# Performance work log

Hardware: AMD Instinct MI355X
Metric: run time of the kernel (lower is better)

Reference implementation:

```python
import jax, jax.numpy as jnp
import numpy as np

D = 1024
H = 16
DH = D // H

def setup_inputs() -> dict:
    key = jax.random.key(0)
    k1, k2, k3, k4 = jax.random.split(key, 4)
    x = jax.random.normal(k1, (4, 2048, D), dtype=jnp.float32)
    # qkv_linear: Linear(D, D, bias=False); weight stored as (out, in) torch-style
    w_qkv = jax.random.normal(k2, (D, D), dtype=jnp.float32) * (1.0 / np.sqrt(D))
    # final linear: Linear(D, D) with bias
    w_out = jax.random.normal(k3, (D, D), dtype=jnp.float32) * (1.0 / np.sqrt(D))
    b_out = jax.random.normal(k4, (D,), dtype=jnp.float32) * 0.01
    return {"x": x, "w_qkv": w_qkv, "w_out": w_out, "b_out": b_out}

def reference(x, w_qkv, w_out, b_out):
    B, S, E = x.shape
    # Same projection used for Q, K, V (faithful to original module)
    qkv = jnp.einsum('bse,de->bsd', x, w_qkv)           # [B,S,D]
    qkv = qkv.reshape(B, S, H, DH).transpose(0, 2, 1, 3)  # [B,H,S,Dh]
    q = k = v = qkv
    scale = DH ** -0.5
    attn = jnp.einsum('bhqd,bhkd->bhqk', q, k) * scale   # [B,H,S,S]
    attn = jax.nn.softmax(attn, axis=-1)
    out = jnp.einsum('bhqk,bhkd->bhqd', attn, v)         # [B,H,S,Dh]
    out = out.transpose(0, 2, 1, 3).reshape(B, S, E)
    return jnp.einsum('bse,de->bsd', out, w_out) + b_out
```

## Files before the change

kernel.cpp:

```cpp
#include <hip/hip_runtime.h>
#include <hip/hip_bf16.h>
#include <stdint.h>

typedef unsigned short u16;
typedef unsigned int   u32;
typedef unsigned long long u64;
typedef __bf16 bf16x8 __attribute__((ext_vector_type(8)));
typedef float  f32x4  __attribute__((ext_vector_type(4)));
typedef short  s16x4  __attribute__((ext_vector_type(4)));

#define D_MODEL 1024
#define NH 16
#define DHEAD 64
#define BB 4
#define SS 2048
#define MM (BB*SS)

__device__ __forceinline__ u16 f2bf(float f) {
    unsigned int u = __float_as_uint(f);
    u += 0x7fffu + ((u >> 16) & 1u);
    return (u16)(u >> 16);
}
__device__ __forceinline__ float bf2f(u16 s) {
    return __uint_as_float(((unsigned int)s) << 16);
}
__device__ __forceinline__ u32 pkbf(float a, float b) {
    __hip_bfloat162 h = __float22bfloat162_rn(make_float2(a, b));
    return *(u32*)&h;
}

union U8 {
    uint4 q;
    u16   v[8];
    bf16x8 f;
};
union B8 { u32 w[4]; bf16x8 f; };
union V8 { s16x4 h[2]; bf16x8 f; };

#define N4X (MM * D_MODEL / 4)
#define N4W (D_MODEL * D_MODEL / 4)
__global__ __launch_bounds__(256) void cvt_all_kernel(const float* __restrict__ x,
                                                      const float* __restrict__ wq,
                                                      const float* __restrict__ wo,
                                                      u16* __restrict__ xb,
                                                      u16* __restrict__ wqb,
                                                      u16* __restrict__ wob) {
    int i = blockIdx.x * 256 + threadIdx.x;
    const float* s; u16* d; int off;
    if (i < N4X)            { s = x;  d = xb;  off = i; }
    else if (i < N4X + N4W) { s = wq; d = wqb; off = i - N4X; }
    else                    { s = wo; d = wob; off = i - N4X - N4W; }
    float4 f = ((const float4*)s)[off];
    u32 o[2] = { pkbf(f.x, f.y), pkbf(f.z, f.w) };
    ((uint2*)d)[off] = *(const uint2*)o;
}

template <bool PERMUTE_OUT>
__device__ __forceinline__ void gemm_body(const u16* __restrict__ A,
                                          const u16* __restrict__ Bt,
                                          const float* __restrict__ Bo,
                                          u16* __restrict__ Cq, u16* __restrict__ CqT,
                                          float* __restrict__ Out)
{
    __shared__ __align__(16) u16 As[128*64];
    __shared__ __align__(16) u16 Bs[128*64];

    const int tid  = threadIdx.x;
    const int wave = tid >> 6;
    const int lane = tid & 63;
    const int quad = lane >> 4;
    const int l16  = lane & 15;
    const int dsw = blockIdx.x;
    const int sl  = dsw >> 3;
    const int bm  = ((sl >> 3) << 3) + (dsw & 7);
    const int bn  = sl & 7;
    const int wm = wave >> 1, wn = wave & 1;

    f32x4 acc[4][4] = {};

    const int rp = tid >> 3;
    const int ch = tid & 7;
    const int sc = ch ^ (rp & 7);

    const u16* Ab = A  + (size_t)(bm * 128 + rp) * D_MODEL + sc * 8;
    const u16* Bb = Bt + (size_t)(bn * 128 + rp) * D_MODEL + sc * 8;
    const int xr = l16 & 7;

    for (int k0 = 0; k0 < D_MODEL; k0 += 64) {
#pragma unroll
        for (int p = 0; p < 4; ++p) {
            __builtin_amdgcn_global_load_lds(
                (__attribute__((address_space(1))) void*)(Ab + (size_t)(32*p) * D_MODEL + k0),
                (__attribute__((address_space(3))) void*)(As + p*2048 + tid*8), 16, 0, 0);
            __builtin_amdgcn_global_load_lds(
                (__attribute__((address_space(1))) void*)(Bb + (size_t)(32*p) * D_MODEL + k0),
                (__attribute__((address_space(3))) void*)(Bs + p*2048 + tid*8), 16, 0, 0);
        }
        __syncthreads();

#pragma unroll
        for (int ks = 0; ks < 2; ++ks) {
            bf16x8 af[4], bfr[4];
#pragma unroll
            for (int t = 0; t < 4; ++t)
                af[t] = *(const bf16x8*)(const void*)(
                    As + (wm*64 + t*16 + l16)*64 + (((ks*4 + quad) ^ xr) * 8));
#pragma unroll
            for (int t = 0; t < 4; ++t)
                bfr[t] = *(const bf16x8*)(const void*)(
                    Bs + (wn*64 + t*16 + l16)*64 + (((ks*4 + quad) ^ xr) * 8));
#pragma unroll
            for (int i = 0; i < 4; ++i)
#pragma unroll
                for (int j = 0; j < 4; ++j)
                    acc[i][j] = __builtin_amdgcn_mfma_f32_16x16x32_bf16(af[i], bfr[j], acc[i][j], 0, 0, 0);
        }
        __syncthreads();
    }

    const int rowbase = bm*128 + wm*64;
    const int colbase = bn*128 + wn*64;
    if (PERMUTE_OUT) {
#pragma unroll
        for (int j = 0; j < 4; ++j) {
            const int col = colbase + j*16 + l16;
            const int h = col >> 6, dh = col & 63;
#pragma unroll
            for (int i = 0; i < 4; ++i) {
                const int row0 = rowbase + i*16 + quad*4;
                const int b = row0 >> 11, s0 = row0 & (SS - 1);
#pragma unroll
                for (int r = 0; r < 4; ++r)
                    Cq[(((size_t)(b*NH + h))*SS + s0 + r)*DHEAD + dh] = f2bf(acc[i][j][r]);
                u64 w = (u64)pkbf(acc[i][j][0], acc[i][j][1])
                      | ((u64)pkbf(acc[i][j][2], acc[i][j][3]) << 32);
                *(u64*)(CqT + ((size_t)((b*NH + h)*DHEAD + dh))*SS + s0) = w;
            }
        }
    } else {
#pragma unroll
        for (int j = 0; j < 4; ++j) {
            const int col = colbase + j*16 + l16;
            const float bias = Bo[col];
#pragma unroll
            for (int i = 0; i < 4; ++i) {
#pragma unroll
                for (int r = 0; r < 4; ++r) {
                    const int row = rowbase + i*16 + quad*4 + r;
                    Out[(size_t)row * D_MODEL + col] = acc[i][j][r] + bias;
                }
            }
        }
    }
}

__global__ __launch_bounds__(256) void gemm_qkv_kernel(const u16* __restrict__ A,
                                                       const u16* __restrict__ Bt,
                                                       u16* __restrict__ Cq,
                                                       u16* __restrict__ CqT) {
    gemm_body<true>(A, Bt, nullptr, Cq, CqT, nullptr);
}

__global__ __launch_bounds__(256) void gemm_out_kernel(const u16* __restrict__ A,
                                                       const u16* __restrict__ Bt,
                                                       const float* __restrict__ Bo,
                                                       float* __restrict__ Out) {
    gemm_body<false>(A, Bt, Bo, nullptr, nullptr, Out);
}

__global__ __launch_bounds__(256, 2) void attn_kernel(const u16* __restrict__ qkv,
                                                      const u16* __restrict__ qkvT,
                                                      u16* __restrict__ outb)
{
    __shared__ __align__(16) u16 Ks[2*2048];
    __shared__ __align__(16) u16 Vt[2*2048];

    const int tid  = threadIdx.x;
    const int wave = tid >> 6;
    const int lane = tid & 63;
    const int quad = lane >> 4;
    const int l16  = lane & 15;

    const int dsw  = blockIdx.x;
    const int sl   = dsw >> 3;
    const int bh   = ((sl >> 3) << 3) + (dsw & 7);
    const int qblk = sl & 7;
    const int b = bh >> 4, h = bh & 15;
    const int qbase = qblk * 256 + wave * 64;

    const u16* Qp = qkv + (size_t)bh * SS * DHEAD;
    const float qscale = 0.125f * 1.4426950408889634f;

    bf16x8 qb[4][2];
#pragma unroll
    for (int nt = 0; nt < 4; ++nt)
#pragma unroll
        for (int ks = 0; ks < 2; ++ks) {
            U8 raw; raw.q = *(const uint4*)(Qp + (size_t)(qbase + nt*16 + l16)*DHEAD + ks*32 + quad*8);
            U8 w;
#pragma unroll
            for (int jj = 0; jj < 4; ++jj)
                ((u32*)&w)[jj] = pkbf(bf2f(raw.v[2*jj]) * qscale, bf2f(raw.v[2*jj+1]) * qscale);
            qb[nt][ks] = w.f;
        }

    const int rK = tid >> 3, cK = (tid & 7) ^ ((rK >> 1) & 7);
    const u16* srcK = qkv  + (size_t)bh * SS * DHEAD + rK * DHEAD + cK * 8;
    const int rV = tid >> 2, cV = (tid & 3) ^ ((rV >> 1) & 3);
    const u16* srcV = qkvT + (size_t)bh * DHEAD * SS + (size_t)rV * SS + cV * 8;

    const int h8 = (l16 >> 1) & 7, h4 = (l16 >> 1) & 3;
    const int ko0 = l16*64 + ((quad)     ^ h8) * 8;
    const int ko1 = l16*64 + ((4 + quad) ^ h8) * 8;
    const int vo0 = l16*32 + (((quad >> 1))     ^ h4) * 8 + (quad & 1) * 4;
    const int vo1 = l16*32 + ((2 + (quad >> 1)) ^ h4) * 8 + (quad & 1) * 4;

    bf16x8 ones;
#pragma unroll
    for (int j = 0; j < 8; ++j) ones[j] = (__bf16)1.0f;

    f32x4 ot[4][4] = {};
    f32x4 lsum[4]  = {};

    __builtin_amdgcn_global_load_lds(
        (__attribute__((address_space(1))) void*)(srcK),
        (__attribute__((address_space(3))) void*)(Ks + tid*8), 16, 0, 0);
    __builtin_amdgcn_global_load_lds(
        (__attribute__((address_space(1))) void*)(srcV),
        (__attribute__((address_space(3))) void*)(Vt + tid*8), 16, 0, 0);

#pragma unroll 2
    for (int kt = 0; kt < SS/32; ++kt) {
        __syncthreads();
        if (kt < SS/32 - 1) {
            __builtin_amdgcn_global_load_lds(
                (__attribute__((address_space(1))) void*)(srcK + (size_t)(kt+1)*32*DHEAD),
                (__attribute__((address_space(3))) void*)(Ks + ((kt+1)&1)*2048 + tid*8), 16, 0, 0);
            __builtin_amdgcn_global_load_lds(
                (__attribute__((address_space(1))) void*)(srcV + (kt+1)*32),
                (__attribute__((address_space(3))) void*)(Vt + ((kt+1)&1)*2048 + tid*8), 16, 0, 0);
        }
        const u16* Kb = Ks + (kt&1)*2048;
        const u16* Vb = Vt + (kt&1)*2048;

        V8 vt[4];
#pragma unroll
        for (int dt = 0; dt < 4; ++dt) {
            vt[dt].h[0] = *(const s16x4*)(const void*)(Vb + dt*512 + vo0);
            vt[dt].h[1] = *(const s16x4*)(const void*)(Vb + dt*512 + vo1);
        }

        B8 pb[4];
#pragma unroll
        for (int mt = 0; mt < 2; ++mt) {
            bf16x8 kf0 = *(const bf16x8*)(const void*)(Kb + mt*1024 + ko0);
            bf16x8 kf1 = *(const bf16x8*)(const void*)(Kb + mt*1024 + ko1);
            f32x4 s[4] = {};
            __builtin_amdgcn_s_setprio(1);
#pragma unroll
            for (int nt = 0; nt < 4; ++nt)
                s[nt] = __builtin_amdgcn_mfma_f32_16x16x32_bf16(kf0, qb[nt][0], s[nt], 0, 0, 0);
#pragma unroll
            for (int nt = 0; nt < 4; ++nt)
                s[nt] = __builtin_amdgcn_mfma_f32_16x16x32_bf16(kf1, qb[nt][1], s[nt], 0, 0, 0);
            __builtin_amdgcn_s_setprio(0);
#pragma unroll
            for (int nt = 0; nt < 4; ++nt) {
                float p0 = __builtin_amdgcn_exp2f(s[nt][0]);
                float p1 = __builtin_amdgcn_exp2f(s[nt][1]);
                float p2 = __builtin_amdgcn_exp2f(s[nt][2]);
                float p3 = __builtin_amdgcn_exp2f(s[nt][3]);
                pb[nt].w[2*mt]   = pkbf(p0, p1);
                pb[nt].w[2*mt+1] = pkbf(p2, p3);
            }
        }

        __builtin_amdgcn_s_setprio(1);
#pragma unroll
        for (int nt = 0; nt < 4; ++nt)
            lsum[nt] = __builtin_amdgcn_mfma_f32_16x16x32_bf16(ones, pb[nt].f, lsum[nt], 0, 0, 0);
#pragma unroll
        for (int dt = 0; dt < 4; ++dt)
#pragma unroll
            for (int nt = 0; nt < 4; ++nt)
                ot[dt][nt] = __builtin_amdgcn_mfma_f32_16x16x32_bf16(vt[dt].f, pb[nt].f, ot[dt][nt], 0, 0, 0);
        __builtin_amdgcn_s_setprio(0);
    }

    float inv[4];
#pragma unroll
    for (int nt = 0; nt < 4; ++nt) inv[nt] = 1.0f / lsum[nt][0];
#pragma unroll
    for (int dt = 0; dt < 4; ++dt)
#pragma unroll
        for (int nt = 0; nt < 4; ++nt) {
            u64 w = (u64)pkbf(ot[dt][nt][0]*inv[nt], ot[dt][nt][1]*inv[nt])
                  | ((u64)pkbf(ot[dt][nt][2]*inv[nt], ot[dt][nt][3]*inv[nt]) << 32);
            *(u64*)(outb + ((size_t)(b*SS + qbase + nt*16 + l16))*D_MODEL
                         + h*64 + dt*16 + quad*4) = w;
        }
}

extern "C" void kernel_launch(void* const* d_in, const int* in_sizes, int n_in,
                              void* d_out, int out_size, void* d_ws, size_t ws_size,
                              hipStream_t stream)
{
    (void)in_sizes; (void)n_in; (void)out_size; (void)ws_size;
    const float* x  = (const float*)d_in[0];
    const float* wq = (const float*)d_in[1];
    const float* wo = (const float*)d_in[2];
    const float* bo = (const float*)d_in[3];

    char* ws = (char*)d_ws;
    u16* xb    = (u16*)(ws);
    u16* wqb   = (u16*)(ws + (size_t)(16 << 20));
    u16* wob   = (u16*)(ws + (size_t)(18 << 20));
    u16* qkvb  = (u16*)(ws + (size_t)(20 << 20));
    u16* qkvTb = (u16*)(ws + (size_t)(36 << 20));
    u16* attb  = xb;

    cvt_all_kernel<<<(N4X + 2*N4W) / 256, 256, 0, stream>>>(x, wq, wo, xb, wqb, wob);
    gemm_qkv_kernel<<<(MM/128) * (D_MODEL/128), 256, 0, stream>>>(xb, wqb, qkvb, qkvTb);
    attn_kernel<<<BB * NH * (SS/256), 256, 0, stream>>>(qkvb, qkvTb, attb);
    gemm_out_kernel<<<(MM/128) * (D_MODEL/128), 256, 0, stream>>>(attb, wob, bo, (float*)d_out);
}
```

Before: 218.9 us.

## Split key sequence across two wave groups per attention block with LDS reduction

Doubles the attention block to 512 threads, with two groups of four waves each processing half of the key/value sequence into separate LDS double buffers. Partial row sums and output accumulators are then combined through shared memory before normalization and store. The aim is more waves in flight per CU and a shorter serial key loop per block. In exchange it adds a cross-group LDS reduction with extra barriers and tighter register pressure from the launch bounds.

```diff
diff --git a/kernel.cpp b/kernel.cpp
--- a/kernel.cpp
+++ b/kernel.cpp
@@ -168,25 +168,29 @@
     gemm_body<false>(A, Bt, Bo, nullptr, nullptr, Out);
 }
 
-__global__ __launch_bounds__(256, 2) void attn_kernel(const u16* __restrict__ qkv,
+__global__ __launch_bounds__(512, 4) void attn_kernel(const u16* __restrict__ qkv,
                                                       const u16* __restrict__ qkvT,
                                                       u16* __restrict__ outb)
 {
-    __shared__ __align__(16) u16 Ks[2*2048];
-    __shared__ __align__(16) u16 Vt[2*2048];
+    __shared__ __align__(16) u16 smem[16384];
+    u16* Ks = smem;
+    u16* Vt = smem + 8192;
 
     const int tid  = threadIdx.x;
     const int wave = tid >> 6;
+    const int grp  = wave >> 2;
+    const int w4   = wave & 3;
     const int lane = tid & 63;
     const int quad = lane >> 4;
     const int l16  = lane & 15;
+    const int t    = tid & 255;
 
     const int dsw  = blockIdx.x;
     const int sl   = dsw >> 3;
     const int bh   = ((sl >> 3) << 3) + (dsw & 7);
     const int qblk = sl & 7;
     const int b = bh >> 4, h = bh & 15;
-    const int qbase = qblk * 256 + wave * 64;
+    const int qbase = qblk * 256 + w4 * 64;
 
     const u16* Qp = qkv + (size_t)bh * SS * DHEAD;
     const float qscale = 0.125f * 1.4426950408889634f;
@@ -204,10 +208,13 @@
             qb[nt][ks] = w.f;
         }
 
-    const int rK = tid >> 3, cK = (tid & 7) ^ ((rK >> 1) & 7);
-    const u16* srcK = qkv  + (size_t)bh * SS * DHEAD + rK * DHEAD + cK * 8;
-    const int rV = tid >> 2, cV = (tid & 3) ^ ((rV >> 1) & 3);
-    const u16* srcV = qkvT + (size_t)bh * DHEAD * SS + (size_t)rV * SS + cV * 8;
+    const int rK = t >> 3, cK = (t & 7) ^ ((rK >> 1) & 7);
+    const u16* srcK = qkv  + (size_t)bh * SS * DHEAD + (size_t)grp*1024*DHEAD + rK * DHEAD + cK * 8;
+    const int rV = t >> 2, cV = (t & 3) ^ ((rV >> 1) & 3);
+    const u16* srcV = qkvT + (size_t)bh * DHEAD * SS + (size_t)rV * SS + grp*1024 + cV * 8;
+
+    u16* KsG = Ks + grp*4096;
+    u16* VtG = Vt + grp*4096;
 
     const int h8 = (l16 >> 1) & 7, h4 = (l16 >> 1) & 3;
     const int ko0 = l16*64 + ((quad)     ^ h8) * 8;
@@ -224,24 +231,24 @@
 
     __builtin_amdgcn_global_load_lds(
         (__attribute__((address_space(1))) void*)(srcK),
-        (__attribute__((address_space(3))) void*)(Ks + tid*8), 16, 0, 0);
+        (__attribute__((address_space(3))) void*)(KsG + t*8), 16, 0, 0);
     __builtin_amdgcn_global_load_lds(
         (__attribute__((address_space(1))) void*)(srcV),
-        (__attribute__((address_space(3))) void*)(Vt + tid*8), 16, 0, 0);
+        (__attribute__((address_space(3))) void*)(VtG + t*8), 16, 0, 0);
 
 #pragma unroll 2
-    for (int kt = 0; kt < SS/32; ++kt) {
-        __syncthreads();
-        if (kt < SS/32 - 1) {
+    for (int kt = 0; kt < SS/64; ++kt) {
+        __syncthreads();
+        if (kt < SS/64 - 1) {
             __builtin_amdgcn_global_load_lds(
                 (__attribute__((address_space(1))) void*)(srcK + (size_t)(kt+1)*32*DHEAD),
-                (__attribute__((address_space(3))) void*)(Ks + ((kt+1)&1)*2048 + tid*8), 16, 0, 0);
+                (__attribute__((address_space(3))) void*)(KsG + ((kt+1)&1)*2048 + t*8), 16, 0, 0);
             __builtin_amdgcn_global_load_lds(
                 (__attribute__((address_space(1))) void*)(srcV + (kt+1)*32),
-                (__attribute__((address_space(3))) void*)(Vt + ((kt+1)&1)*2048 + tid*8), 16, 0, 0);
-        }
-        const u16* Kb = Ks + (kt&1)*2048;
-        const u16* Vb = Vt + (kt&1)*2048;
+                (__attribute__((address_space(3))) void*)(VtG + ((kt+1)&1)*2048 + t*8), 16, 0, 0);
+        }
+        const u16* Kb = KsG + (kt&1)*2048;
+        const u16* Vb = VtG + (kt&1)*2048;
 
         V8 vt[4];
 #pragma unroll
@@ -287,18 +294,49 @@
         __builtin_amdgcn_s_setprio(0);
     }
 
+    __syncthreads();
+    float* ex = (float*)smem;
+
+    if (grp == 0) {
+#pragma unroll
+        for (int nt = 0; nt < 4; ++nt) ex[(w4*64 + lane)*4 + nt] = lsum[nt][0];
+    }
+    __syncthreads();
     float inv[4];
-#pragma unroll
-    for (int nt = 0; nt < 4; ++nt) inv[nt] = 1.0f / lsum[nt][0];
-#pragma unroll
-    for (int dt = 0; dt < 4; ++dt)
-#pragma unroll
-        for (int nt = 0; nt < 4; ++nt) {
-            u64 w = (u64)pkbf(ot[dt][nt][0]*inv[nt], ot[dt][nt][1]*inv[nt])
-                  | ((u64)pkbf(ot[dt][nt][2]*inv[nt], ot[dt][nt][3]*inv[nt]) << 32);
-            *(u64*)(outb + ((size_t)(b*SS + qbase + nt*16 + l16))*D_MODEL
-                         + h*64 + dt*16 + quad*4) = w;
-        }
+    if (grp == 1) {
+#pragma unroll
+        for (int nt = 0; nt < 4; ++nt)
+            inv[nt] = 1.0f / (lsum[nt][0] + ex[(w4*64 + lane)*4 + nt]);
+    }
+    __syncthreads();
+
+#pragma unroll
+    for (int dt = 0; dt < 4; ++dt) {
+        if (grp == 0) {
+            f32x4* dst = (f32x4*)ex + (w4*64 + lane)*4;
+#pragma unroll
+            for (int nt = 0; nt < 4; ++nt) dst[nt] = ot[dt][nt];
+        }
+        __syncthreads();
+        if (grp == 1) {
+            const f32x4* src = (const f32x4*)ex + (w4*64 + lane)*4;
+#pragma unroll
+            for (int nt = 0; nt < 4; ++nt) ot[dt][nt] += src[nt];
+        }
+        __syncthreads();
+    }
+
+    if (grp == 1) {
+#pragma unroll
+        for (int dt = 0; dt < 4; ++dt)
+#pragma unroll
+            for (int nt = 0; nt < 4; ++nt) {
+                u64 w = (u64)pkbf(ot[dt][nt][0]*inv[nt], ot[dt][nt][1]*inv[nt])
+                      | ((u64)pkbf(ot[dt][nt][2]*inv[nt], ot[dt][nt][3]*inv[nt]) << 32);
+                *(u64*)(outb + ((size_t)(b*SS + qbase + nt*16 + l16))*D_MODEL
+                             + h*64 + dt*16 + quad*4) = w;
+            }
+    }
 }
 
 extern "C" void kernel_launch(void* const* d_in, const int* in_sizes, int n_in,
@@ -321,6 +359,6 @@
 
     cvt_all_kernel<<<(N4X + 2*N4W) / 256, 256, 0, stream>>>(x, wq, wo, xb, wqb, wob);
     gemm_qkv_kernel<<<(MM/128) * (D_MODEL/128), 256, 0, stream>>>(xb, wqb, qkvb, qkvTb);
-    attn_kernel<<<BB * NH * (SS/256), 256, 0, stream>>>(qkvb, qkvTb, attb);
+    attn_kernel<<<BB * NH * (SS/256), 512, 0, stream>>>(qkvb, qkvTb, attb);
     gemm_out_kernel<<<(MM/128) * (D_MODEL/128), 256, 0, stream>>>(attb, wob, bo, (float*)d_out);
 }
```

New measurement: 694.8 us. +217.4%, slower.

## Software-pipeline attention loop with 4-stage LDS ring and skewed QK/PV

Applied to the files above, without the earlier changes.

Replaces the double-buffered K/V staging with a four-slot LDS ring that keeps up to three tiles in flight, using explicit vmcnt waits plus a barrier instead of __syncthreads. The loop is skewed so each iteration issues the QK^T MFMAs for tile kt+1 before the PV MFMAs for tile kt, and computes that tile's exp2 afterwards. This lets transcendental and conversion work overlap with matrix ops and hides more global-load latency. In exchange it doubles LDS use, which may limit occupancy at two blocks per CU, and raises register pressure from holding s and pb across iterations.

```diff
diff --git a/kernel.cpp b/kernel.cpp
--- a/kernel.cpp
+++ b/kernel.cpp
@@ -172,8 +172,8 @@
                                                       const u16* __restrict__ qkvT,
                                                       u16* __restrict__ outb)
 {
-    __shared__ __align__(16) u16 Ks[2*2048];
-    __shared__ __align__(16) u16 Vt[2*2048];
+    __shared__ __align__(16) u16 Ks[4*2048];
+    __shared__ __align__(16) u16 Vt[4*2048];
 
     const int tid  = threadIdx.x;
     const int wave = tid >> 6;
@@ -221,27 +221,58 @@
 
     f32x4 ot[4][4] = {};
     f32x4 lsum[4]  = {};
-
-    __builtin_amdgcn_global_load_lds(
-        (__attribute__((address_space(1))) void*)(srcK),
-        (__attribute__((address_space(3))) void*)(Ks + tid*8), 16, 0, 0);
-    __builtin_amdgcn_global_load_lds(
-        (__attribute__((address_space(1))) void*)(srcV),
-        (__attribute__((address_space(3))) void*)(Vt + tid*8), 16, 0, 0);
-
-#pragma unroll 2
-    for (int kt = 0; kt < SS/32; ++kt) {
-        __syncthreads();
-        if (kt < SS/32 - 1) {
-            __builtin_amdgcn_global_load_lds(
-                (__attribute__((address_space(1))) void*)(srcK + (size_t)(kt+1)*32*DHEAD),
-                (__attribute__((address_space(3))) void*)(Ks + ((kt+1)&1)*2048 + tid*8), 16, 0, 0);
-            __builtin_amdgcn_global_load_lds(
-                (__attribute__((address_space(1))) void*)(srcV + (kt+1)*32),
-                (__attribute__((address_space(3))) void*)(Vt + ((kt+1)&1)*2048 + tid*8), 16, 0, 0);
-        }
-        const u16* Kb = Ks + (kt&1)*2048;
-        const u16* Vb = Vt + (kt&1)*2048;
+    B8 pb[4];
+
+    auto issue = [&](int t) {
+        __builtin_amdgcn_global_load_lds(
+            (__attribute__((address_space(1))) void*)(srcK + (size_t)t*32*DHEAD),
+            (__attribute__((address_space(3))) void*)(Ks + (t&3)*2048 + tid*8), 16, 0, 0);
+        __builtin_amdgcn_global_load_lds(
+            (__attribute__((address_space(1))) void*)(srcV + t*32),
+            (__attribute__((address_space(3))) void*)(Vt + (t&3)*2048 + tid*8), 16, 0, 0);
+    };
+
+    issue(0); issue(1); issue(2);
+    asm volatile("s_waitcnt vmcnt(4) lgkmcnt(0)\n\ts_barrier" ::: "memory");
+    {
+        const u16* Kb = Ks;
+        f32x4 s[2][4];
+#pragma unroll
+        for (int mt = 0; mt < 2; ++mt) {
+            bf16x8 kf0 = *(const bf16x8*)(const void*)(Kb + mt*1024 + ko0);
+            bf16x8 kf1 = *(const bf16x8*)(const void*)(Kb + mt*1024 + ko1);
+#pragma unroll
+            for (int nt = 0; nt < 4; ++nt) {
+                f32x4 z = {};
+                z = __builtin_amdgcn_mfma_f32_16x16x32_bf16(kf0, qb[nt][0], z, 0, 0, 0);
+                s[mt][nt] = __builtin_amdgcn_mfma_f32_16x16x32_bf16(kf1, qb[nt][1], z, 0, 0, 0);
+            }
+        }
+#pragma unroll
+        for (int nt = 0; nt < 4; ++nt) {
+#pragma unroll
+            for (int mt = 0; mt < 2; ++mt) {
+                float p0 = __builtin_amdgcn_exp2f(s[mt][nt][0]);
+                float p1 = __builtin_amdgcn_exp2f(s[mt][nt][1]);
+                float p2 = __builtin_amdgcn_exp2f(s[mt][nt][2]);
+                float p3 = __builtin_amdgcn_exp2f(s[mt][nt][3]);
+                pb[nt].w[2*mt]   = pkbf(p0, p1);
+                pb[nt].w[2*mt+1] = pkbf(p2, p3);
+            }
+        }
+    }
+
+    for (int kt = 0; kt < SS/32 - 1; ++kt) {
+        if (kt < SS/32 - 3) {
+            asm volatile("s_waitcnt vmcnt(2) lgkmcnt(0)\n\ts_barrier" ::: "memory");
+            issue(kt + 3);
+        } else if (kt == SS/32 - 3) {
+            asm volatile("s_waitcnt vmcnt(2) lgkmcnt(0)\n\ts_barrier" ::: "memory");
+        } else {
+            asm volatile("s_waitcnt vmcnt(0) lgkmcnt(0)\n\ts_barrier" ::: "memory");
+        }
+        const u16* Kb = Ks + ((kt+1)&3)*2048;
+        const u16* Vb = Vt + (kt&3)*2048;
 
         V8 vt[4];
 #pragma unroll
@@ -249,32 +280,56 @@
             vt[dt].h[0] = *(const s16x4*)(const void*)(Vb + dt*512 + vo0);
             vt[dt].h[1] = *(const s16x4*)(const void*)(Vb + dt*512 + vo1);
         }
-
-        B8 pb[4];
+        bf16x8 kf[2][2];
 #pragma unroll
         for (int mt = 0; mt < 2; ++mt) {
-            bf16x8 kf0 = *(const bf16x8*)(const void*)(Kb + mt*1024 + ko0);
-            bf16x8 kf1 = *(const bf16x8*)(const void*)(Kb + mt*1024 + ko1);
-            f32x4 s[4] = {};
-            __builtin_amdgcn_s_setprio(1);
+            kf[mt][0] = *(const bf16x8*)(const void*)(Kb + mt*1024 + ko0);
+            kf[mt][1] = *(const bf16x8*)(const void*)(Kb + mt*1024 + ko1);
+        }
+
+        f32x4 s[2][4];
+        __builtin_amdgcn_s_setprio(1);
+#pragma unroll
+        for (int mt = 0; mt < 2; ++mt)
+#pragma unroll
+            for (int nt = 0; nt < 4; ++nt) {
+                f32x4 z = {};
+                z = __builtin_amdgcn_mfma_f32_16x16x32_bf16(kf[mt][0], qb[nt][0], z, 0, 0, 0);
+                s[mt][nt] = __builtin_amdgcn_mfma_f32_16x16x32_bf16(kf[mt][1], qb[nt][1], z, 0, 0, 0);
+            }
+
+#pragma unroll
+        for (int nt = 0; nt < 4; ++nt)
+            lsum[nt] = __builtin_amdgcn_mfma_f32_16x16x32_bf16(ones, pb[nt].f, lsum[nt], 0, 0, 0);
+#pragma unroll
+        for (int dt = 0; dt < 4; ++dt)
 #pragma unroll
             for (int nt = 0; nt < 4; ++nt)
-                s[nt] = __builtin_amdgcn_mfma_f32_16x16x32_bf16(kf0, qb[nt][0], s[nt], 0, 0, 0);
-#pragma unroll
-            for (int nt = 0; nt < 4; ++nt)
-                s[nt] = __builtin_amdgcn_mfma_f32_16x16x32_bf16(kf1, qb[nt][1], s[nt], 0, 0, 0);
-            __builtin_amdgcn_s_setprio(0);
-#pragma unroll
-            for (int nt = 0; nt < 4; ++nt) {
-                float p0 = __builtin_amdgcn_exp2f(s[nt][0]);
-                float p1 = __builtin_amdgcn_exp2f(s[nt][1]);
-                float p2 = __builtin_amdgcn_exp2f(s[nt][2]);
-                float p3 = __builtin_amdgcn_exp2f(s[nt][3]);
+                ot[dt][nt] = __builtin_amdgcn_mfma_f32_16x16x32_bf16(vt[dt].f, pb[nt].f, ot[dt][nt], 0, 0, 0);
+        __builtin_amdgcn_s_setprio(0);
+
+#pragma unroll
+        for (int nt = 0; nt < 4; ++nt) {
+#pragma unroll
+            for (int mt = 0; mt < 2; ++mt) {
+                float p0 = __builtin_amdgcn_exp2f(s[mt][nt][0]);
+                float p1 = __builtin_amdgcn_exp2f(s[mt][nt][1]);
+                float p2 = __builtin_amdgcn_exp2f(s[mt][nt][2]);
+                float p3 = __builtin_amdgcn_exp2f(s[mt][nt][3]);
                 pb[nt].w[2*mt]   = pkbf(p0, p1);
                 pb[nt].w[2*mt+1] = pkbf(p2, p3);
             }
         }
-
+    }
+
+    {
+        const u16* Vb = Vt + ((SS/32 - 1)&3)*2048;
+        V8 vt[4];
+#pragma unroll
+        for (int dt = 0; dt < 4; ++dt) {
+            vt[dt].h[0] = *(const s16x4*)(const void*)(Vb + dt*512 + vo0);
+            vt[dt].h[1] = *(const s16x4*)(const void*)(Vb + dt*512 + vo1);
+        }
         __builtin_amdgcn_s_setprio(1);
 #pragma unroll
         for (int nt = 0; nt < 4; ++nt)
```

New measurement: 220.0 us. No clear change (+0.5%).

## Halve attention query tile and double K/V stage size per barrier

Applied to the files above, without the earlier changes.

The attention kernel now gives each block 128 queries (32 per wave) instead of 256, doubling the grid and the occupancy target to 4 blocks per CU. Each pipeline stage loads 64 keys instead of 32, so there is one barrier per two sub-tiles, with an explicit waitcnt plus barrier. The intent is more parallelism and fewer synchronisations. In exchange, each wave reuses each K/V tile across fewer queries, so total K/V traffic from global memory and LDS doubles, and LDS use per block doubles.

```diff
diff --git a/kernel.cpp b/kernel.cpp
--- a/kernel.cpp
+++ b/kernel.cpp
@@ -168,12 +168,12 @@
     gemm_body<false>(A, Bt, Bo, nullptr, nullptr, Out);
 }
 
-__global__ __launch_bounds__(256, 2) void attn_kernel(const u16* __restrict__ qkv,
+__global__ __launch_bounds__(256, 4) void attn_kernel(const u16* __restrict__ qkv,
                                                       const u16* __restrict__ qkvT,
                                                       u16* __restrict__ outb)
 {
-    __shared__ __align__(16) u16 Ks[2*2048];
-    __shared__ __align__(16) u16 Vt[2*2048];
+    __shared__ __align__(16) u16 Ks[2*2*2048];
+    __shared__ __align__(16) u16 Vt[2*2*2048];
 
     const int tid  = threadIdx.x;
     const int wave = tid >> 6;
@@ -183,17 +183,17 @@
 
     const int dsw  = blockIdx.x;
     const int sl   = dsw >> 3;
-    const int bh   = ((sl >> 3) << 3) + (dsw & 7);
-    const int qblk = sl & 7;
+    const int bh   = ((sl >> 4) << 3) + (dsw & 7);
+    const int qblk = sl & 15;
     const int b = bh >> 4, h = bh & 15;
-    const int qbase = qblk * 256 + wave * 64;
+    const int qbase = qblk * 128 + wave * 32;
 
     const u16* Qp = qkv + (size_t)bh * SS * DHEAD;
     const float qscale = 0.125f * 1.4426950408889634f;
 
-    bf16x8 qb[4][2];
-#pragma unroll
-    for (int nt = 0; nt < 4; ++nt)
+    bf16x8 qb[2][2];
+#pragma unroll
+    for (int nt = 0; nt < 2; ++nt)
 #pragma unroll
         for (int ks = 0; ks < 2; ++ks) {
             U8 raw; raw.q = *(const uint4*)(Qp + (size_t)(qbase + nt*16 + l16)*DHEAD + ks*32 + quad*8);
@@ -219,53 +219,51 @@
 #pragma unroll
     for (int j = 0; j < 8; ++j) ones[j] = (__bf16)1.0f;
 
-    f32x4 ot[4][4] = {};
-    f32x4 lsum[4]  = {};
-
-    __builtin_amdgcn_global_load_lds(
-        (__attribute__((address_space(1))) void*)(srcK),
-        (__attribute__((address_space(3))) void*)(Ks + tid*8), 16, 0, 0);
-    __builtin_amdgcn_global_load_lds(
-        (__attribute__((address_space(1))) void*)(srcV),
-        (__attribute__((address_space(3))) void*)(Vt + tid*8), 16, 0, 0);
-
-#pragma unroll 2
-    for (int kt = 0; kt < SS/32; ++kt) {
-        __syncthreads();
-        if (kt < SS/32 - 1) {
-            __builtin_amdgcn_global_load_lds(
-                (__attribute__((address_space(1))) void*)(srcK + (size_t)(kt+1)*32*DHEAD),
-                (__attribute__((address_space(3))) void*)(Ks + ((kt+1)&1)*2048 + tid*8), 16, 0, 0);
-            __builtin_amdgcn_global_load_lds(
-                (__attribute__((address_space(1))) void*)(srcV + (kt+1)*32),
-                (__attribute__((address_space(3))) void*)(Vt + ((kt+1)&1)*2048 + tid*8), 16, 0, 0);
-        }
-        const u16* Kb = Ks + (kt&1)*2048;
-        const u16* Vb = Vt + (kt&1)*2048;
-
+    f32x4 ot[4][2] = {};
+    f32x4 lsum[2]  = {};
+
+    auto issue = [&](int it) {
+        u16* kb = Ks + (it&1)*4096;
+        u16* vb = Vt + (it&1)*4096;
+        const u16* sk = srcK + (size_t)it*64*DHEAD;
+        const u16* sv = srcV + it*64;
+        __builtin_amdgcn_global_load_lds(
+            (__attribute__((address_space(1))) void*)(sk),
+            (__attribute__((address_space(3))) void*)(kb + tid*8), 16, 0, 0);
+        __builtin_amdgcn_global_load_lds(
+            (__attribute__((address_space(1))) void*)(sk + 32*DHEAD),
+            (__attribute__((address_space(3))) void*)(kb + 2048 + tid*8), 16, 0, 0);
+        __builtin_amdgcn_global_load_lds(
+            (__attribute__((address_space(1))) void*)(sv),
+            (__attribute__((address_space(3))) void*)(vb + tid*8), 16, 0, 0);
+        __builtin_amdgcn_global_load_lds(
+            (__attribute__((address_space(1))) void*)(sv + 32),
+            (__attribute__((address_space(3))) void*)(vb + 2048 + tid*8), 16, 0, 0);
+    };
+
+    auto sub = [&](const u16* Kb, const u16* Vb) {
         V8 vt[4];
 #pragma unroll
         for (int dt = 0; dt < 4; ++dt) {
             vt[dt].h[0] = *(const s16x4*)(const void*)(Vb + dt*512 + vo0);
             vt[dt].h[1] = *(const s16x4*)(const void*)(Vb + dt*512 + vo1);
         }
-
-        B8 pb[4];
+        B8 pb[2];
 #pragma unroll
         for (int mt = 0; mt < 2; ++mt) {
             bf16x8 kf0 = *(const bf16x8*)(const void*)(Kb + mt*1024 + ko0);
             bf16x8 kf1 = *(const bf16x8*)(const void*)(Kb + mt*1024 + ko1);
-            f32x4 s[4] = {};
+            f32x4 s[2] = {};
             __builtin_amdgcn_s_setprio(1);
 #pragma unroll
-            for (int nt = 0; nt < 4; ++nt)
+            for (int nt = 0; nt < 2; ++nt)
                 s[nt] = __builtin_amdgcn_mfma_f32_16x16x32_bf16(kf0, qb[nt][0], s[nt], 0, 0, 0);
 #pragma unroll
-            for (int nt = 0; nt < 4; ++nt)
+            for (int nt = 0; nt < 2; ++nt)
                 s[nt] = __builtin_amdgcn_mfma_f32_16x16x32_bf16(kf1, qb[nt][1], s[nt], 0, 0, 0);
             __builtin_amdgcn_s_setprio(0);
 #pragma unroll
-            for (int nt = 0; nt < 4; ++nt) {
+            for (int nt = 0; nt < 2; ++nt) {
                 float p0 = __builtin_amdgcn_exp2f(s[nt][0]);
                 float p1 = __builtin_amdgcn_exp2f(s[nt][1]);
                 float p2 = __builtin_amdgcn_exp2f(s[nt][2]);
@@ -274,26 +272,36 @@
                 pb[nt].w[2*mt+1] = pkbf(p2, p3);
             }
         }
-
         __builtin_amdgcn_s_setprio(1);
 #pragma unroll
-        for (int nt = 0; nt < 4; ++nt)
+        for (int nt = 0; nt < 2; ++nt)
             lsum[nt] = __builtin_amdgcn_mfma_f32_16x16x32_bf16(ones, pb[nt].f, lsum[nt], 0, 0, 0);
 #pragma unroll
         for (int dt = 0; dt < 4; ++dt)
 #pragma unroll
-            for (int nt = 0; nt < 4; ++nt)
+            for (int nt = 0; nt < 2; ++nt)
                 ot[dt][nt] = __builtin_amdgcn_mfma_f32_16x16x32_bf16(vt[dt].f, pb[nt].f, ot[dt][nt], 0, 0, 0);
         __builtin_amdgcn_s_setprio(0);
+    };
+
+    issue(0);
+
+    for (int it = 0; it < SS/64; ++it) {
+        asm volatile("s_waitcnt vmcnt(0) lgkmcnt(0)\n\ts_barrier" ::: "memory");
+        if (it < SS/64 - 1) issue(it + 1);
+        const u16* Kb = Ks + (it&1)*4096;
+        const u16* Vb = Vt + (it&1)*4096;
+        sub(Kb, Vb);
+        sub(Kb + 2048, Vb + 2048);
     }
 
-    float inv[4];
-#pragma unroll
-    for (int nt = 0; nt < 4; ++nt) inv[nt] = 1.0f / lsum[nt][0];
+    float inv[2];
+#pragma unroll
+    for (int nt = 0; nt < 2; ++nt) inv[nt] = 1.0f / lsum[nt][0];
 #pragma unroll
     for (int dt = 0; dt < 4; ++dt)
 #pragma unroll
-        for (int nt = 0; nt < 4; ++nt) {
+        for (int nt = 0; nt < 2; ++nt) {
             u64 w = (u64)pkbf(ot[dt][nt][0]*inv[nt], ot[dt][nt][1]*inv[nt])
                   | ((u64)pkbf(ot[dt][nt][2]*inv[nt], ot[dt][nt][3]*inv[nt]) << 32);
             *(u64*)(outb + ((size_t)(b*SS + qbase + nt*16 + l16))*D_MODEL
@@ -321,6 +329,6 @@
 
     cvt_all_kernel<<<(N4X + 2*N4W) / 256, 256, 0, stream>>>(x, wq, wo, xb, wqb, wob);
     gemm_qkv_kernel<<<(MM/128) * (D_MODEL/128), 256, 0, stream>>>(xb, wqb, qkvb, qkvTb);
-    attn_kernel<<<BB * NH * (SS/256), 256, 0, stream>>>(qkvb, qkvTb, attb);
+    attn_kernel<<<BB * NH * (SS/128), 256, 0, stream>>>(qkvb, qkvTb, attb);
     gemm_out_kernel<<<(MM/128) * (D_MODEL/128), 256, 0, stream>>>(attb, wob, bo, (float*)d_out);
 }
```

After: 219.5 us. Within noise of the previous version (+0.3%).
